# Kernel tuning notes

Hardware: AMD Instinct MI355X
Metric: run time of the kernel (lower is better)

The kernel has to match this reference:

```python
import jax, jax.numpy as jnp
import numpy as np

# dims
B, NB, T, NC = 16, 55, 512, 8          # batch, filter bands, time steps, CSP comps
D, L, H, E, K, F, C = 512, 6, 8, 8, 2, 2048, 2  # embed, depth, heads, experts, top_k, d_ff, classes
DH = D // H
IN = NB * NC  # 440
EPS = 1e-5


def _ln(x, s, b):
    m = x.mean(-1, keepdims=True)
    v = ((x - m) ** 2).mean(-1, keepdims=True)
    return (x - m) / jnp.sqrt(v + EPS) * s + b


def setup_inputs() -> dict:
    key = jax.random.key(0)
    ks = iter(jax.random.split(key, 64))
    n = lambda shape, s=0.02: jax.random.normal(next(ks), shape, jnp.float32) * s
    inp = {
        "x": jax.random.normal(next(ks), (B, NB, T, NC), jnp.float32),
        # frontend
        "proj_w": n((IN, D)), "proj_b": jnp.zeros((D,), jnp.float32),
        "pos": n((1, T, D)),
        "ln_pre_s": jnp.ones((D,), jnp.float32), "ln_pre_b": jnp.zeros((D,), jnp.float32),
        # stacked transformer-block params [L, ...]
        "ln1_s": jnp.ones((L, D), jnp.float32), "ln1_b": jnp.zeros((L, D), jnp.float32),
        "wq": n((L, D, D)), "bq": jnp.zeros((L, D), jnp.float32),
        "wk": n((L, D, D)), "bk": jnp.zeros((L, D), jnp.float32),
        "wv": n((L, D, D)), "bv": jnp.zeros((L, D), jnp.float32),
        "wo": n((L, D, D)), "bo": jnp.zeros((L, D), jnp.float32),
        "ln2_s": jnp.ones((L, D), jnp.float32), "ln2_b": jnp.zeros((L, D), jnp.float32),
        "gate_w": n((L, D, E)),
        "e_w1": n((L, E, D, F)), "e_b1": jnp.zeros((L, E, F), jnp.float32),
        "e_w2": n((L, E, F, D)), "e_b2": jnp.zeros((L, E, D), jnp.float32),
        # classifier head
        "ln_f_s": jnp.ones((D,), jnp.float32), "ln_f_b": jnp.zeros((D,), jnp.float32),
        "head_w": n((D, C)), "head_b": jnp.zeros((C,), jnp.float32),
    }
    return inp


def _moe(h, gw, w1, b1, w2, b2):
    # h: [N, D]; top-K softmax-gated mixture of GELU-FFN experts + load-balance aux loss
    N = h.shape[0]
    probs = jax.nn.softmax(h @ gw, axis=-1)                  # [N, E]
    vals, idx = jax.lax.top_k(probs, K)                      # [N, K]
    w = vals / vals.sum(-1, keepdims=True)                   # renormalized top-k weights
    disp = jax.nn.one_hot(idx, E, dtype=h.dtype)             # [N, K, E]
    combine = (disp * w[..., None]).sum(1)                   # [N, E]
    y = jnp.zeros_like(h)
    for e in range(E):  # small fixed expert loop
        y = y + combine[:, e:e + 1] * (jax.nn.gelu(h @ w1[e] + b1[e]) @ w2[e] + b2[e])
    frac = disp.mean((0, 1)) * K                             # fraction of tokens routed to each expert
    aux = E * jnp.sum(frac * probs.mean(0))
    return y, aux


def reference(x, proj_w, proj_b, pos, ln_pre_s, ln_pre_b, ln1_s, ln1_b, wq, bq, wk, bk,
              wv, bv, wo, bo, ln2_s, ln2_b, gate_w, e_w1, e_b1, e_w2, e_b2,
              ln_f_s, ln_f_b, head_w, head_b):
    b, nb, t, nc = x.shape
    h = x.transpose(0, 2, 1, 3).reshape(b, t, nb * nc) @ proj_w + proj_b  # [B,T,D]
    h = _ln(h + pos[:, :t, :], ln_pre_s, ln_pre_b)
    scale = DH ** -0.5
    total_aux = jnp.float32(0.0)
    for l in range(L):
        # pre-LN multi-head self-attention
        a = _ln(h, ln1_s[l], ln1_b[l])
        q = (a @ wq[l] + bq[l]).reshape(b, t, H, DH)
        k = (a @ wk[l] + bk[l]).reshape(b, t, H, DH)
        v = (a @ wv[l] + bv[l]).reshape(b, t, H, DH)
        att = jax.nn.softmax(jnp.einsum('bqhd,bkhd->bhqk', q, k) * scale, axis=-1)
        o = jnp.einsum('bhqk,bkhd->bqhd', att, v).reshape(b, t, D) @ wo[l] + bo[l]
        h = h + o
        # pre-LN MoE FFN
        m = _ln(h, ln2_s[l], ln2_b[l]).reshape(b * t, D)
        y, aux = _moe(m, gate_w[l], e_w1[l], e_b1[l], e_w2[l], e_b2[l])
        h = h + y.reshape(b, t, D)
        total_aux = total_aux + aux
    pooled = h.mean(axis=1)                                   # [B, D]
    logits = _ln(pooled, ln_f_s, ln_f_b) @ head_w + head_b    # [B, C]
    return logits, total_aux
```

## Files before the change

### kernel.cpp

```cpp
#include <hip/hip_runtime.h>
#include <stdint.h>

typedef unsigned short u16;
typedef unsigned int   u32;
typedef short bh8 __attribute__((ext_vector_type(8)));
typedef float f4  __attribute__((ext_vector_type(4)));

#define NTOK    8192
#define PADROWS 17408
#define MAXTILES 136

__device__ __forceinline__ u16 f2bf(float f){
  u32 u = __float_as_uint(f);
  return (u16)((u + 0x7fffu + ((u>>16)&1u)) >> 16);
}
__device__ __forceinline__ float bf2f(u16 h){ return __uint_as_float(((u32)h)<<16); }
__device__ __forceinline__ u32 pk2(float a, float b){ return (u32)f2bf(a) | ((u32)f2bf(b)<<16); }
__device__ __forceinline__ float gelu_f(float x){
  float u = 0.7978845608028654f*(x + 0.044715f*x*x*x);
  float t = 1.f - 2.f/(__expf(2.f*u)+1.f);
  return 0.5f*x*(1.f+t);
}
__device__ __forceinline__ void gload_lds16(const void* g, void* l){
  __builtin_amdgcn_global_load_lds((const __attribute__((address_space(1))) u32*)g,
                                   (__attribute__((address_space(3))) u32*)l, 16, 0, 0);
}

__global__ __launch_bounds__(256) void xpose_k(const float* __restrict__ x, u16* __restrict__ xt){
  int idx = blockIdx.x*256 + threadIdx.x;
  const float* src = x + (size_t)idx*8;
  float4 a = *(const float4*)src;
  float4 b = *(const float4*)(src+4);
  int t  = idx & 511;
  int nb = (idx>>9) % 55;
  int bb = (idx>>9) / 55;
  uint4 u;
  u.x = pk2(a.x,a.y); u.y = pk2(a.z,a.w); u.z = pk2(b.x,b.y); u.w = pk2(b.z,b.w);
  *(uint4*)&xt[((size_t)(bb*512+t))*448 + nb*8] = u;
}

__device__ __forceinline__ void tile_xpose(const float* __restrict__ src, u16* __restrict__ dst,
                                           int Ksrc, int N, int Kdst, float (*tile)[65])
{
  int tid = threadIdx.x;
  int k0 = blockIdx.y*64, n0 = blockIdx.x*64;
  #pragma unroll
  for (int p=0;p<4;++p){
    int r = p*16 + (tid>>4);
    int c4 = (tid&15)*4;
    int k = k0 + r;
    float4 v = (k < Ksrc) ? *(const float4*)&src[(size_t)k*N + n0 + c4] : (float4){0.f,0.f,0.f,0.f};
    tile[r][c4]=v.x; tile[r][c4+1]=v.y; tile[r][c4+2]=v.z; tile[r][c4+3]=v.w;
  }
  __syncthreads();
  #pragma unroll
  for (int p=0;p<2;++p){
    int rn = p*32 + (tid>>3);
    int ck = (tid&7)*8;
    uint4 u;
    u.x = pk2(tile[ck+0][rn], tile[ck+1][rn]);
    u.y = pk2(tile[ck+2][rn], tile[ck+3][rn]);
    u.z = pk2(tile[ck+4][rn], tile[ck+5][rn]);
    u.w = pk2(tile[ck+6][rn], tile[ck+7][rn]);
    *(uint4*)&dst[(size_t)(n0+rn)*Kdst + k0 + ck] = u;
  }
}

__global__ __launch_bounds__(256) void wconv_k(const float* __restrict__ src, u16* __restrict__ dst,
                                               int Ksrc, int N, int Kdst){
  __shared__ float tile[64][65];
  src += (size_t)blockIdx.z*Ksrc*N;
  dst += (size_t)blockIdx.z*N*Kdst;
  tile_xpose(src, dst, Ksrc, N, Kdst, tile);
}

__global__ __launch_bounds__(256) void wconvqkvo_k(const float* __restrict__ wq, const float* __restrict__ wk,
    const float* __restrict__ wv, const float* __restrict__ wo,
    u16* __restrict__ qkvt, u16* __restrict__ wot)
{
  __shared__ float tile[64][65];
  int z = blockIdx.z;
  int l = z>>2, which = z&3;
  const float* src = ((which==0)? wq : (which==1)? wk : (which==2)? wv : wo) + (size_t)l*512*512;
  u16* dst = (which==3) ? wot + (size_t)l*512*512
                        : qkvt + (size_t)l*1536*512 + (size_t)which*512*512;
  tile_xpose(src, dst, 512, 512, 512, tile);
}

__global__ __launch_bounds__(256) void qkvb_k(const float* __restrict__ bq, const float* __restrict__ bk,
                                              const float* __restrict__ bv, float* __restrict__ qkvb){
  int idx = blockIdx.x*256 + threadIdx.x;
  int l = idx/1536, c = idx - l*1536;
  const float* s = (c<512)? bq : (c<1024)? bk : bv;
  qkvb[idx] = s[l*512 + (c&511)];
}

template<int MODE, bool GATHER>
__global__ __launch_bounds__(256) void gemm2_k(
    const u16* __restrict__ A, int lda,
    const u16* __restrict__ Bt, int ldb, int Ksteps,
    const float* __restrict__ biasBase,
    float* __restrict__ Cf, u16* __restrict__ Cb, int ldc,
    const int* __restrict__ tile_e, const int* __restrict__ toklist,
    const float* __restrict__ wlist, int expN)
{
  __shared__ __align__(16) u16 SMEM[17408];
  u16* As_ = SMEM;
  u16* Bs_ = SMEM + 8192;
  const int tid = threadIdx.x, lane = tid&63, w = tid>>6;
  const int wr = w>>1, wc = w&1;
  int nx = gridDim.x;
  int nwg = nx * gridDim.y;
  int lin = blockIdx.y*nx + blockIdx.x;
  int qq = nwg>>3, rr = nwg&7, xc = lin&7, oo = lin>>3;
  int wg = (xc<rr ? xc*(qq+1) : rr*(qq+1)+(xc-rr)*qq) + oo;
  int by = wg/nx, bx = wg - by*nx;
  const int n0 = bx*128, m0 = by*128;
  const u16* Bp = Bt;
  const float* bias = biasBase;
  if constexpr (MODE>=3){
    int e = tile_e[by];
    Bp   += (size_t)e*(size_t)expN*(size_t)ldb;
    bias += (size_t)e*(size_t)expN;
  }
  const u16* asrc0; const u16* asrc1; const u16* bsrc0; const u16* bsrc1;
  {
    int idx0 = tid, row0 = idx0>>2, sp0 = idx0&3, ks0 = sp0 ^ ((row0>>1)&3);
    int idx1 = 256+tid, row1 = idx1>>2, sp1 = idx1&3, ks1 = sp1 ^ ((row1>>1)&3);
    size_t ar0 = GATHER ? (size_t)toklist[m0+row0] : (size_t)(m0+row0);
    size_t ar1 = GATHER ? (size_t)toklist[m0+row1] : (size_t)(m0+row1);
    asrc0 = A + ar0*(size_t)lda + ks0*8;
    asrc1 = A + ar1*(size_t)lda + ks1*8;
    bsrc0 = Bp + (size_t)(n0+row0)*ldb + ks0*8;
    bsrc1 = Bp + (size_t)(n0+row1)*ldb + ks1*8;
  }
  f4 acc[4][4];
  #pragma unroll
  for (int i=0;i<4;++i)
    #pragma unroll
    for (int j=0;j<4;++j) acc[i][j] = (f4){0.f,0.f,0.f,0.f};

  gload_lds16(asrc0, &As_[tid*8]);
  gload_lds16(asrc1, &As_[(256+tid)*8]);
  gload_lds16(bsrc0, &Bs_[tid*8]);
  gload_lds16(bsrc1, &Bs_[(256+tid)*8]);
  asrc0 += 32; asrc1 += 32; bsrc0 += 32; bsrc1 += 32;
  __syncthreads();

  int buf = 0;
  for (int kt=0; kt<Ksteps; ++kt){
    if (kt+1 < Ksteps){
      int nb = buf^1;
      gload_lds16(asrc0, &As_[nb*4096 + tid*8]);
      gload_lds16(asrc1, &As_[nb*4096 + (256+tid)*8]);
      gload_lds16(bsrc0, &Bs_[nb*4096 + tid*8]);
      gload_lds16(bsrc1, &Bs_[nb*4096 + (256+tid)*8]);
      asrc0 += 32; asrc1 += 32; bsrc0 += 32; bsrc1 += 32;
    }
    bh8 af[4], bf[4];
    const int q = lane>>4;
    #pragma unroll
    for (int mf=0;mf<4;++mf){
      int r = wr*64 + mf*16 + (lane&15);
      af[mf] = *(const bh8*)&As_[buf*4096 + r*32 + (q ^ ((r>>1)&3))*8];
    }
    #pragma unroll
    for (int nf=0;nf<4;++nf){
      int r = wc*64 + nf*16 + (lane&15);
      bf[nf] = *(const bh8*)&Bs_[buf*4096 + r*32 + (q ^ ((r>>1)&3))*8];
    }
    #pragma unroll
    for (int mf=0;mf<4;++mf)
      #pragma unroll
      for (int nf=0;nf<4;++nf)
        acc[mf][nf] = __builtin_amdgcn_mfma_f32_16x16x32_bf16(af[mf], bf[nf], acc[mf][nf], 0, 0, 0);
    __syncthreads();
    buf ^= 1;
  }
  if constexpr (MODE==1 || MODE==3 || MODE==4){
    u16* Cs = SMEM;
    #pragma unroll
    for (int mf=0;mf<4;++mf){
      int row0 = wr*64 + mf*16 + (lane>>4)*4;
      float wl[4];
      if constexpr (MODE==4){
        #pragma unroll
        for (int r=0;r<4;++r) wl[r] = wlist[m0+row0+r];
      }
      #pragma unroll
      for (int nf=0;nf<4;++nf){
        f4 d = acc[mf][nf];
        int col = wc*64 + nf*16 + (lane&15);
        float bv = bias[n0+col];
        #pragma unroll
        for (int r=0;r<4;++r){
          float val = d[r] + bv;
          if constexpr (MODE==3) val = gelu_f(val);
          if constexpr (MODE==4) val = wl[r]*val;
          Cs[(row0+r)*136 + col] = f2bf(val);
        }
      }
    }
    __syncthreads();
    #pragma unroll
    for (int p=0;p<8;++p){
      int idx = p*256 + tid;
      int row = idx>>4, c4 = idx&15;
      bh8 v = *(const bh8*)&Cs[row*136 + c4*8];
      int mrow = m0 + row;
      if constexpr (MODE==1){
        int nc = n0 + c4*8;
        int slab = nc>>6, dh = nc&63;
        *(bh8*)&Cb[((size_t)slab*NTOK + (size_t)mrow)*64 + dh] = v;
      } else {
        *(bh8*)&Cb[(size_t)mrow*ldc + n0 + c4*8] = v;
      }
    }
  } else {
    #pragma unroll
    for (int mf=0;mf<4;++mf){
      #pragma unroll
      for (int nf=0;nf<4;++nf){
        f4 d = acc[mf][nf];
        int ncol = n0 + wc*64 + nf*16 + (lane&15);
        float bv = bias[ncol];
        #pragma unroll
        for (int r=0;r<4;++r){
          int mrow = m0 + wr*64 + mf*16 + (lane>>4)*4 + r;
          float val = d[r] + bv;
          if constexpr (MODE==0){
            Cf[(size_t)mrow*ldc + ncol] = val;
          } else {
            Cf[(size_t)mrow*ldc + ncol] += val;
          }
        }
      }
    }
  }
}

template<bool ADDPOS, bool OUTF32>
__global__ __launch_bounds__(256) void ln_k(const float* __restrict__ X, const float* __restrict__ pos,
    const float* __restrict__ sc, const float* __restrict__ bi,
    float* __restrict__ outF, u16* __restrict__ outB)
{
  int tid=threadIdx.x, lane=tid&63, w=tid>>6;
  int row = blockIdx.x*4 + w;
  const float* xr = X + (size_t)row*512 + lane*8;
  float x[8];
  float4 v0 = *(const float4*)xr;
  float4 v1 = *(const float4*)(xr+4);
  x[0]=v0.x;x[1]=v0.y;x[2]=v0.z;x[3]=v0.w;x[4]=v1.x;x[5]=v1.y;x[6]=v1.z;x[7]=v1.w;
  if constexpr (ADDPOS){
    const float* pr = pos + (size_t)(row&511)*512 + lane*8;
    float4 p0 = *(const float4*)pr, p1 = *(const float4*)(pr+4);
    x[0]+=p0.x;x[1]+=p0.y;x[2]+=p0.z;x[3]+=p0.w;x[4]+=p1.x;x[5]+=p1.y;x[6]+=p1.z;x[7]+=p1.w;
  }
  float sm=0.f, sq=0.f;
  #pragma unroll
  for (int i=0;i<8;++i){ sm+=x[i]; sq+=x[i]*x[i]; }
  #pragma unroll
  for (int mk=1; mk<64; mk<<=1){ sm += __shfl_xor(sm, mk); sq += __shfl_xor(sq, mk); }
  float mean = sm*(1.f/512.f);
  float var  = sq*(1.f/512.f) - mean*mean;
  float rstd = rsqrtf(var + 1e-5f);
  int d0 = lane*8;
  float4 s0 = *(const float4*)(sc+d0), s1 = *(const float4*)(sc+d0+4);
  float4 b0 = *(const float4*)(bi+d0), b1 = *(const float4*)(bi+d0+4);
  float y[8];
  y[0]=(x[0]-mean)*rstd*s0.x+b0.x; y[1]=(x[1]-mean)*rstd*s0.y+b0.y;
  y[2]=(x[2]-mean)*rstd*s0.z+b0.z; y[3]=(x[3]-mean)*rstd*s0.w+b0.w;
  y[4]=(x[4]-mean)*rstd*s1.x+b1.x; y[5]=(x[5]-mean)*rstd*s1.y+b1.y;
  y[6]=(x[6]-mean)*rstd*s1.z+b1.z; y[7]=(x[7]-mean)*rstd*s1.w+b1.w;
  if constexpr (OUTF32){
    float4 o0 = {y[0],y[1],y[2],y[3]}, o1 = {y[4],y[5],y[6],y[7]};
    *(float4*)(outF + (size_t)row*512 + d0)     = o0;
    *(float4*)(outF + (size_t)row*512 + d0 + 4) = o1;
  } else {
    uint4 u; u.x=pk2(y[0],y[1]); u.y=pk2(y[2],y[3]); u.z=pk2(y[4],y[5]); u.w=pk2(y[6],y[7]);
    *(uint4*)&outB[(size_t)row*512 + d0] = u;
  }
}

__global__ __launch_bounds__(256) void gatherln_k(float* __restrict__ h,
    const u16* __restrict__ yb, const int* __restrict__ t2pos,
    const float* __restrict__ sc, const float* __restrict__ bi, u16* __restrict__ outB)
{
  int tid=threadIdx.x, lane=tid&63, w=tid>>6;
  int row = blockIdx.x*4 + w;
  float* hp = h + (size_t)row*512 + lane*8;
  float4 v0 = *(float4*)hp, v1 = *(float4*)(hp+4);
  int p0 = t2pos[2*row], p1 = t2pos[2*row+1];
  uint4 ya = *(const uint4*)&yb[(size_t)p0*512 + lane*8];
  uint4 yv = *(const uint4*)&yb[(size_t)p1*512 + lane*8];
  float x[8];
  x[0]=v0.x + bf2f((u16)(ya.x&0xffff)) + bf2f((u16)(yv.x&0xffff));
  x[1]=v0.y + bf2f((u16)(ya.x>>16))    + bf2f((u16)(yv.x>>16));
  x[2]=v0.z + bf2f((u16)(ya.y&0xffff)) + bf2f((u16)(yv.y&0xffff));
  x[3]=v0.w + bf2f((u16)(ya.y>>16))    + bf2f((u16)(yv.y>>16));
  x[4]=v1.x + bf2f((u16)(ya.z&0xffff)) + bf2f((u16)(yv.z&0xffff));
  x[5]=v1.y + bf2f((u16)(ya.z>>16))    + bf2f((u16)(yv.z>>16));
  x[6]=v1.z + bf2f((u16)(ya.w&0xffff)) + bf2f((u16)(yv.w&0xffff));
  x[7]=v1.w + bf2f((u16)(ya.w>>16))    + bf2f((u16)(yv.w>>16));
  float4 o0 = {x[0],x[1],x[2],x[3]}, o1 = {x[4],x[5],x[6],x[7]};
  *(float4*)hp = o0; *(float4*)(hp+4) = o1;
  float sm=0.f, sq=0.f;
  #pragma unroll
  for (int i=0;i<8;++i){ sm+=x[i]; sq+=x[i]*x[i]; }
  #pragma unroll
  for (int mk=1; mk<64; mk<<=1){ sm += __shfl_xor(sm, mk); sq += __shfl_xor(sq, mk); }
  float mean = sm*(1.f/512.f);
  float rstd = rsqrtf(sq*(1.f/512.f) - mean*mean + 1e-5f);
  int d0 = lane*8;
  float4 s0 = *(const float4*)(sc+d0), s1 = *(const float4*)(sc+d0+4);
  float4 b0 = *(const float4*)(bi+d0), b1 = *(const float4*)(bi+d0+4);
  float y[8];
  y[0]=(x[0]-mean)*rstd*s0.x+b0.x; y[1]=(x[1]-mean)*rstd*s0.y+b0.y;
  y[2]=(x[2]-mean)*rstd*s0.z+b0.z; y[3]=(x[3]-mean)*rstd*s0.w+b0.w;
  y[4]=(x[4]-mean)*rstd*s1.x+b1.x; y[5]=(x[5]-mean)*rstd*s1.y+b1.y;
  y[6]=(x[6]-mean)*rstd*s1.z+b1.z; y[7]=(x[7]-mean)*rstd*s1.w+b1.w;
  uint4 u; u.x=pk2(y[0],y[1]); u.y=pk2(y[2],y[3]); u.z=pk2(y[4],y[5]); u.w=pk2(y[6],y[7]);
  *(uint4*)&outB[(size_t)row*512 + d0] = u;
}

__global__ __launch_bounds__(256) void attn_k(const u16* __restrict__ QKV, u16* __restrict__ Og)
{
  __shared__ __align__(16) u16 VT[2][64*72];
  __shared__ __align__(16) u16 PS[4][16*72];
  int tid=threadIdx.x, lane=tid&63, w=tid>>6;
  int qt=blockIdx.x, hh=blockIdx.y, bb=blockIdx.z;
  const u16* Qh = QKV + ((size_t)hh     *NTOK + (size_t)bb*512)*64;
  const u16* Kh = QKV + ((size_t)(8+hh) *NTOK + (size_t)bb*512)*64;
  const u16* Vh = QKV + ((size_t)(16+hh)*NTOK + (size_t)bb*512)*64;
  size_t obase = (size_t)bb*512*512 + (size_t)hh*64;
  int qrow0 = qt*64 + w*16;
  bh8 qf[2];
  #pragma unroll
  for (int kf=0;kf<2;++kf)
    qf[kf] = *(const bh8*)&Qh[ (size_t)(qrow0 + (lane&15))*64 + kf*32 + (lane>>4)*8 ];
  f4 oacc[4];
  #pragma unroll
  for (int i=0;i<4;++i) oacc[i] = (f4){0.f,0.f,0.f,0.f};
  float mrun[4] = {-1e30f,-1e30f,-1e30f,-1e30f};
  float lrun[4] = {0.f,0.f,0.f,0.f};
  const float scale = 0.125f;

  for (int kt=0; kt<8; ++kt){
    const int buf = kt&1;
    #pragma unroll
    for (int r2=0;r2<2;++r2){
      int idx = r2*256 + tid;
      int dhg = idx&7;
      int dh0 = dhg*8, key = idx>>3;
      uint4 raw = *(const uint4*)&Vh[ (size_t)(kt*64+key)*64 + dh0 ];
      int kx = key ^ (dhg<<3);
      u32 rw[4] = {raw.x, raw.y, raw.z, raw.w};
      #pragma unroll
      for (int j=0;j<4;++j){
        VT[buf][(dh0+2*j  )*72 + kx] = (u16)(rw[j]&0xffff);
        VT[buf][(dh0+2*j+1)*72 + kx] = (u16)(rw[j]>>16);
      }
    }
    f4 s[4];
    #pragma unroll
    for (int nf=0;nf<4;++nf){
      size_t krow = (size_t)(kt*64+nf*16+(lane&15))*64 + (lane>>4)*8;
      bh8 k0 = *(const bh8*)&Kh[krow];
      bh8 k1 = *(const bh8*)&Kh[krow+32];
      f4 z = (f4){0.f,0.f,0.f,0.f};
      z = __builtin_amdgcn_mfma_f32_16x16x32_bf16(qf[0], k0, z, 0,0,0);
      z = __builtin_amdgcn_mfma_f32_16x16x32_bf16(qf[1], k1, z, 0,0,0);
      s[nf] = z;
    }
    float pe[4][4];
    #pragma unroll
    for (int r=0;r<4;++r){
      float sv0=s[0][r]*scale, sv1=s[1][r]*scale, sv2=s[2][r]*scale, sv3=s[3][r]*scale;
      float mt = fmaxf(fmaxf(sv0,sv1), fmaxf(sv2,sv3));
      #pragma unroll
      for (int mk=1; mk<16; mk<<=1) mt = fmaxf(mt, __shfl_xor(mt, mk));
      float mn = fmaxf(mrun[r], mt);
      float sf = __expf(mrun[r]-mn);
      float p0=__expf(sv0-mn), p1=__expf(sv1-mn), p2=__expf(sv2-mn), p3=__expf(sv3-mn);
      pe[0][r]=p0; pe[1][r]=p1; pe[2][r]=p2; pe[3][r]=p3;
      float rs = p0+p1+p2+p3;
      #pragma unroll
      for (int mk=1; mk<16; mk<<=1) rs += __shfl_xor(rs, mk);
      lrun[r] = lrun[r]*sf + rs;
      mrun[r] = mn;
      #pragma unroll
      for (int df=0;df<4;++df) oacc[df][r] *= sf;
    }
    #pragma unroll
    for (int nf=0;nf<4;++nf)
      #pragma unroll
      for (int r=0;r<4;++r)
        PS[w][ ((lane>>4)*4+r)*72 + nf*16 + (lane&15) ] = f2bf(pe[nf][r]);
    __syncthreads();
    #pragma unroll
    for (int ks=0;ks<2;++ks){
      bh8 pa = *(const bh8*)&PS[w][ (lane&15)*72 + ks*32 + (lane>>4)*8 ];
      #pragma unroll
      for (int df=0;df<4;++df){
        int dh = df*16 + (lane&15);
        int sgrp = (dh>>3)&7;
        bh8 vb = *(const bh8*)&VT[buf][ dh*72 + ((ks*4 + (lane>>4)) ^ sgrp)*8 ];
        oacc[df] = __builtin_amdgcn_mfma_f32_16x16x32_bf16(pa, vb, oacc[df], 0,0,0);
      }
    }
  }
  #pragma unroll
  for (int df=0;df<4;++df)
    #pragma unroll
    for (int r=0;r<4;++r){
      int qr = qrow0 + (lane>>4)*4 + r;
      float ov = oacc[df][r] / lrun[r];
      Og[ obase + (size_t)qr*512 + df*16 + (lane&15) ] = f2bf(ov);
    }
}

__global__ __launch_bounds__(256) void lnroute_k(const float* __restrict__ h,
    const float* __restrict__ sc, const float* __restrict__ bi, u16* __restrict__ outB,
    const float* __restrict__ gw,
    float* __restrict__ psum, int* __restrict__ cnt, int* __restrict__ t2e, float* __restrict__ t2w)
{
  __shared__ float ps[8]; __shared__ int cs[8];
  int tid=threadIdx.x, lane=tid&63, w=tid>>6;
  if (tid<8){ ps[tid]=0.f; cs[tid]=0; }
  __syncthreads();
  int d0 = lane*8;
  float4 s0 = *(const float4*)(sc+d0), s1 = *(const float4*)(sc+d0+4);
  float4 b0 = *(const float4*)(bi+d0), b1 = *(const float4*)(bi+d0+4);
  for (int it=0; it<4; ++it){
    int t = blockIdx.x*16 + w*4 + it;
    const float* xr = h + (size_t)t*512 + d0;
    float x[8];
    float4 v0 = *(const float4*)xr, v1 = *(const float4*)(xr+4);
    x[0]=v0.x;x[1]=v0.y;x[2]=v0.z;x[3]=v0.w;x[4]=v1.x;x[5]=v1.y;x[6]=v1.z;x[7]=v1.w;
    float sm=0.f, sq=0.f;
    #pragma unroll
    for (int i=0;i<8;++i){ sm+=x[i]; sq+=x[i]*x[i]; }
    #pragma unroll
    for (int mk=1; mk<64; mk<<=1){ sm += __shfl_xor(sm, mk); sq += __shfl_xor(sq, mk); }
    float mean = sm*(1.f/512.f);
    float rstd = rsqrtf(sq*(1.f/512.f) - mean*mean + 1e-5f);
    float y[8];
    y[0]=(x[0]-mean)*rstd*s0.x+b0.x; y[1]=(x[1]-mean)*rstd*s0.y+b0.y;
    y[2]=(x[2]-mean)*rstd*s0.z+b0.z; y[3]=(x[3]-mean)*rstd*s0.w+b0.w;
    y[4]=(x[4]-mean)*rstd*s1.x+b1.x; y[5]=(x[5]-mean)*rstd*s1.y+b1.y;
    y[6]=(x[6]-mean)*rstd*s1.z+b1.z; y[7]=(x[7]-mean)*rstd*s1.w+b1.w;
    uint4 u; u.x=pk2(y[0],y[1]); u.y=pk2(y[2],y[3]); u.z=pk2(y[4],y[5]); u.w=pk2(y[6],y[7]);
    *(uint4*)&outB[(size_t)t*512 + d0] = u;
    float acc[8] = {0,0,0,0,0,0,0,0};
    #pragma unroll
    for (int j=0;j<8;++j){
      const float* g = gw + (size_t)(d0+j)*8;
      float4 g0 = *(const float4*)g, g1 = *(const float4*)(g+4);
      acc[0]+=y[j]*g0.x; acc[1]+=y[j]*g0.y; acc[2]+=y[j]*g0.z; acc[3]+=y[j]*g0.w;
      acc[4]+=y[j]*g1.x; acc[5]+=y[j]*g1.y; acc[6]+=y[j]*g1.z; acc[7]+=y[j]*g1.w;
    }
    #pragma unroll
    for (int mk=1; mk<64; mk<<=1)
      #pragma unroll
      for (int e=0;e<8;++e) acc[e] += __shfl_xor(acc[e], mk);
    if (lane==0){
      float mx=acc[0];
      #pragma unroll
      for (int e=1;e<8;++e) mx = fmaxf(mx, acc[e]);
      float pe[8], tot=0.f;
      #pragma unroll
      for (int e=0;e<8;++e){ pe[e]=__expf(acc[e]-mx); tot+=pe[e]; }
      float inv = 1.f/tot;
      #pragma unroll
      for (int e=0;e<8;++e) pe[e]*=inv;
      int e0=0; float v0e=pe[0];
      #pragma unroll
      for (int e=1;e<8;++e) if (pe[e]>v0e){ v0e=pe[e]; e0=e; }
      int e1=-1; float v1e=-1.f;
      #pragma unroll
      for (int e=0;e<8;++e) if (e!=e0 && pe[e]>v1e){ v1e=pe[e]; e1=e; }
      float invw = 1.f/(v0e+v1e);
      t2e[2*t]=e0; t2w[2*t]=v0e*invw; t2e[2*t+1]=e1; t2w[2*t+1]=v1e*invw;
      #pragma unroll
      for (int e=0;e<8;++e) atomicAdd(&ps[e], pe[e]);
      atomicAdd(&cs[e0],1); atomicAdd(&cs[e1],1);
    }
  }
  __syncthreads();
  if (tid<8){ atomicAdd(&psum[tid], ps[tid]); atomicAdd(&cnt[tid], cs[tid]); }
}

__global__ __launch_bounds__(256) void offsets_k(const int* __restrict__ cnt, const float* __restrict__ psum,
    int* __restrict__ offs, int* __restrict__ fill, int* __restrict__ tile_e,
    int* __restrict__ toklist, float* __restrict__ wlist, float* __restrict__ auxp)
{
  int tid = threadIdx.x, b = blockIdx.x;
  int i = b*256 + tid;
  if (i < PADROWS){ toklist[i]=0; wlist[i]=0.f; }
  if (b==0){
    if (tid==0){
      int off=0; float auxl=0.f;
      for (int e=0;e<8;++e){
        offs[e] = off;
        int reg = (cnt[e]+127)&~127;
        int t0 = off>>7, t1 = (off+reg)>>7;
        for (int t=t0;t<t1;++t) tile_e[t]=e;
        off += reg;
        auxl += ((float)cnt[e]*(1.f/8192.f)) * (psum[e]*(1.f/8192.f));
      }
      for (int t=off>>7; t<MAXTILES; ++t) tile_e[t]=0;
      auxp[0] += 8.f*auxl;
    }
    if (tid<8) fill[tid]=0;
  }
}

__global__ __launch_bounds__(256) void scatter_k(const int* __restrict__ t2e, const float* __restrict__ t2w,
    const int* __restrict__ offs, int* __restrict__ fill,
    int* __restrict__ toklist, float* __restrict__ wlist, int* __restrict__ t2pos)
{
  int t = blockIdx.x*256 + threadIdx.x;
  #pragma unroll
  for (int kk=0;kk<2;++kk){
    int e = t2e[2*t+kk];
    int p = atomicAdd(&fill[e], 1);
    int i = offs[e] + p;
    toklist[i] = t; wlist[i] = t2w[2*t+kk]; t2pos[2*t+kk] = i;
  }
}

__global__ __launch_bounds__(256) void gather_k(float* __restrict__ h, const u16* __restrict__ yb,
                                                const int* __restrict__ t2pos)
{
  int tid = threadIdx.x;
  int t = blockIdx.x*4 + (tid>>6);
  int lane = tid&63;
  int p0 = t2pos[2*t], p1 = t2pos[2*t+1];
  uint4 a = *(const uint4*)&yb[(size_t)p0*512 + lane*8];
  uint4 b = *(const uint4*)&yb[(size_t)p1*512 + lane*8];
  float* hp = h + (size_t)t*512 + lane*8;
  float4 h0 = *(float4*)hp, h1 = *(float4*)(hp+4);
  h0.x += bf2f((u16)(a.x&0xffff)) + bf2f((u16)(b.x&0xffff));
  h0.y += bf2f((u16)(a.x>>16))    + bf2f((u16)(b.x>>16));
  h0.z += bf2f((u16)(a.y&0xffff)) + bf2f((u16)(b.y&0xffff));
  h0.w += bf2f((u16)(a.y>>16))    + bf2f((u16)(b.y>>16));
  h1.x += bf2f((u16)(a.z&0xffff)) + bf2f((u16)(b.z&0xffff));
  h1.y += bf2f((u16)(a.z>>16))    + bf2f((u16)(b.z>>16));
  h1.z += bf2f((u16)(a.w&0xffff)) + bf2f((u16)(b.w&0xffff));
  h1.w += bf2f((u16)(a.w>>16))    + bf2f((u16)(b.w>>16));
  *(float4*)hp = h0; *(float4*)(hp+4) = h1;
}

__global__ __launch_bounds__(256) void pool_k(const float* __restrict__ h, float* __restrict__ pooled){
  int idx = blockIdx.x*256 + threadIdx.x;
  int bb = idx>>9, d = idx&511;
  const float* p = h + (size_t)bb*512*512 + d;
  float s=0.f;
  for (int t=0;t<512;++t) s += p[(size_t)t*512];
  pooled[idx] = s*(1.f/512.f);
}

__global__ __launch_bounds__(256) void head_k(const float* __restrict__ pooled,
    const float* __restrict__ sc, const float* __restrict__ bi,
    const float* __restrict__ hw, const float* __restrict__ hb,
    const float* __restrict__ auxp, float* __restrict__ out)
{
  int tid=threadIdx.x, lane=tid&63, w=tid>>6;
  for (int i=0;i<4;++i){
    int row = w*4+i;
    const float* xr = pooled + (size_t)row*512 + lane*8;
    float x[8];
    float4 v0 = *(const float4*)xr, v1 = *(const float4*)(xr+4);
    x[0]=v0.x;x[1]=v0.y;x[2]=v0.z;x[3]=v0.w;x[4]=v1.x;x[5]=v1.y;x[6]=v1.z;x[7]=v1.w;
    float sm=0.f, sq=0.f;
    #pragma unroll
    for (int j=0;j<8;++j){ sm+=x[j]; sq+=x[j]*x[j]; }
    #pragma unroll
    for (int mk=1; mk<64; mk<<=1){ sm += __shfl_xor(sm, mk); sq += __shfl_xor(sq, mk); }
    float mean = sm*(1.f/512.f);
    float rstd = rsqrtf(sq*(1.f/512.f) - mean*mean + 1e-5f);
    int d0 = lane*8;
    float c0=0.f, c1=0.f;
    #pragma unroll
    for (int j=0;j<8;++j){
      float yv = (x[j]-mean)*rstd*sc[d0+j] + bi[d0+j];
      c0 += yv*hw[(d0+j)*2]; c1 += yv*hw[(d0+j)*2+1];
    }
    #pragma unroll
    for (int mk=1; mk<64; mk<<=1){ c0 += __shfl_xor(c0, mk); c1 += __shfl_xor(c1, mk); }
    if (lane==0){ out[row*2+0] = c0 + hb[0]; out[row*2+1] = c1 + hb[1]; }
  }
  if (tid==0) out[32] = auxp[0];
}

extern "C" void kernel_launch(void* const* d_in, const int* in_sizes, int n_in,
                              void* d_out, int out_size, void* d_ws, size_t ws_size,
                              hipStream_t stream)
{
  (void)in_sizes; (void)n_in; (void)out_size; (void)ws_size;
  const float* x      = (const float*)d_in[0];
  const float* proj_w = (const float*)d_in[1];
  const float* proj_b = (const float*)d_in[2];
  const float* pos    = (const float*)d_in[3];
  const float* ln_pre_s=(const float*)d_in[4];
  const float* ln_pre_b=(const float*)d_in[5];
  const float* ln1_s  = (const float*)d_in[6];
  const float* ln1_b  = (const float*)d_in[7];
  const float* wq     = (const float*)d_in[8];
  const float* bq     = (const float*)d_in[9];
  const float* wk     = (const float*)d_in[10];
  const float* bk     = (const float*)d_in[11];
  const float* wv     = (const float*)d_in[12];
  const float* bv     = (const float*)d_in[13];
  const float* wo     = (const float*)d_in[14];
  const float* bo     = (const float*)d_in[15];
  const float* ln2_s  = (const float*)d_in[16];
  const float* ln2_b  = (const float*)d_in[17];
  const float* gate_w = (const float*)d_in[18];
  const float* e_w1   = (const float*)d_in[19];
  const float* e_b1   = (const float*)d_in[20];
  const float* e_w2   = (const float*)d_in[21];
  const float* e_b2   = (const float*)d_in[22];
  const float* ln_f_s = (const float*)d_in[23];
  const float* ln_f_b = (const float*)d_in[24];
  const float* head_w = (const float*)d_in[25];
  const float* head_b = (const float*)d_in[26];

  char* base = (char*)d_ws;
  size_t off = 0;
  auto carve = [&](size_t bytes)->char*{
    char* r = base + off; off += (bytes + 255) & ~(size_t)255; return r;
  };
  u16*   xt      = (u16*)  carve((size_t)8192*448*2);
  float* h       = (float*)carve((size_t)8192*512*4);
  u16*   a       = (u16*)  carve((size_t)8192*512*2);
  u16*   qkv     = (u16*)  carve((size_t)8192*1536*2);
  u16*   ob      = (u16*)  carve((size_t)8192*512*2);
  u16*   hidden  = (u16*)  carve((size_t)PADROWS*2048*2);
  u16*   ybuf    = (u16*)  carve((size_t)PADROWS*512*2);
  u16*   projt   = (u16*)  carve((size_t)512*448*2);
  u16*   qkvt    = (u16*)  carve((size_t)6*1536*512*2);
  u16*   wot     = (u16*)  carve((size_t)6*512*512*2);
  u16*   w1t     = (u16*)  carve((size_t)6*8*2048*512*2);
  u16*   w2t     = (u16*)  carve((size_t)6*8*512*2048*2);
  float* qkvb    = (float*)carve((size_t)6*1536*4);
  int*   toklist = (int*)  carve(PADROWS*4);
  float* wlist   = (float*)carve(PADROWS*4);
  int*   tile_e  = (int*)  carve(256*4);
  int*   rcntA   = (int*)  carve(6*16*4);
  int*   fill    = (int*)  carve(64);
  int*   offs    = (int*)  carve(64);
  int*   t2e     = (int*)  carve(16384*4);
  float* t2w     = (float*)carve(16384*4);
  int*   t2pos   = (int*)  carve(16384*4);
  float* pooled  = (float*)carve(8192*4);
  float* auxp    = (float*)carve(256);

  hipMemsetAsync(xt, 0, (size_t)8192*448*2, stream);
  hipMemsetAsync(rcntA, 0, 6*16*4, stream);
  hipMemsetAsync(auxp, 0, 4, stream);

  xpose_k<<<1760, 256, 0, stream>>>(x, xt);
  wconv_k<<<dim3(8,7,1), 256, 0, stream>>>(proj_w, projt, 440, 512, 448);
  wconvqkvo_k<<<dim3(8,8,24), 256, 0, stream>>>(wq, wk, wv, wo, qkvt, wot);
  wconv_k<<<dim3(32,8,48), 256, 0, stream>>>(e_w1, w1t, 512, 2048, 512);
  wconv_k<<<dim3(8,32,48), 256, 0, stream>>>(e_w2, w2t, 2048, 512, 2048);
  qkvb_k<<<36, 256, 0, stream>>>(bq, bk, bv, qkvb);
  gemm2_k<0,false><<<dim3(4,64), 256, 0, stream>>>(xt, 448, projt, 448, 14, proj_b,
      h, nullptr, 512, nullptr, nullptr, nullptr, 0);
  ln_k<true,true><<<2048, 256, 0, stream>>>(h, pos, ln_pre_s, ln_pre_b, h, nullptr);

  for (int l=0; l<6; ++l){
    int*   cnt  = rcntA + l*16;
    float* psum = (float*)(cnt + 8);
    if (l == 0)
      ln_k<false,false><<<2048, 256, 0, stream>>>(h, nullptr, ln1_s, ln1_b, nullptr, a);
    else
      gatherln_k<<<2048, 256, 0, stream>>>(h, ybuf, t2pos,
          ln1_s+(size_t)l*512, ln1_b+(size_t)l*512, a);
    gemm2_k<1,false><<<dim3(12,64), 256, 0, stream>>>(a, 512, qkvt+(size_t)l*1536*512, 512, 16,
        qkvb+(size_t)l*1536, nullptr, qkv, 1536, nullptr, nullptr, nullptr, 0);
    attn_k<<<dim3(8,8,16), 256, 0, stream>>>(qkv, ob);
    gemm2_k<2,false><<<dim3(4,64), 256, 0, stream>>>(ob, 512, wot+(size_t)l*512*512, 512, 16,
        bo+(size_t)l*512, h, nullptr, 512, nullptr, nullptr, nullptr, 0);
    lnroute_k<<<512, 256, 0, stream>>>(h, ln2_s+(size_t)l*512, ln2_b+(size_t)l*512, a,
        gate_w+(size_t)l*512*8, psum, cnt, t2e, t2w);
    offsets_k<<<68, 256, 0, stream>>>(cnt, psum, offs, fill, tile_e, toklist, wlist, auxp);
    scatter_k<<<32, 256, 0, stream>>>(t2e, t2w, offs, fill, toklist, wlist, t2pos);
    gemm2_k<3,true ><<<dim3(16,MAXTILES), 256, 0, stream>>>(a, 512, w1t+(size_t)l*8*2048*512, 512, 16,
        e_b1 + (size_t)l*8*2048, nullptr, hidden, 2048, tile_e, toklist, wlist, 2048);
    gemm2_k<4,false><<<dim3(4,MAXTILES), 256, 0, stream>>>(hidden, 2048, w2t+(size_t)l*8*512*2048, 2048, 64,
        e_b2 + (size_t)l*8*512, nullptr, ybuf, 512, tile_e, nullptr, wlist, 512);
  }

  gather_k<<<2048, 256, 0, stream>>>(h, ybuf, t2pos);
  pool_k<<<32, 256, 0, stream>>>(h, pooled);
  head_k<<<1, 256, 0, stream>>>(pooled, ln_f_s, ln_f_b, head_w, head_b, auxp, (float*)d_out);
}
```

Measured before the change: 2.185 ms.

## Switch GEMM k-loop to three-stage LDS pipeline with explicit vmcnt waits

```diff
diff --git a/kernel.cpp b/kernel.cpp
--- a/kernel.cpp
+++ b/kernel.cpp
@@ -104,9 +104,7 @@
     const int* __restrict__ tile_e, const int* __restrict__ toklist,
     const float* __restrict__ wlist, int expN)
 {
-  __shared__ __align__(16) u16 SMEM[17408];
-  u16* As_ = SMEM;
-  u16* Bs_ = SMEM + 8192;
+  __shared__ __align__(16) u16 SMEM[24576];
   const int tid = threadIdx.x, lane = tid&63, w = tid>>6;
   const int wr = w>>1, wc = w&1;
   int nx = gridDim.x;
@@ -140,44 +138,52 @@
     #pragma unroll
     for (int j=0;j<4;++j) acc[i][j] = (f4){0.f,0.f,0.f,0.f};
 
-  gload_lds16(asrc0, &As_[tid*8]);
-  gload_lds16(asrc1, &As_[(256+tid)*8]);
-  gload_lds16(bsrc0, &Bs_[tid*8]);
-  gload_lds16(bsrc1, &Bs_[(256+tid)*8]);
-  asrc0 += 32; asrc1 += 32; bsrc0 += 32; bsrc1 += 32;
-  __syncthreads();
-
-  int buf = 0;
+  auto STAGE = [&](int kt){
+    u16* bufA = SMEM + (kt%3)*8192;
+    u16* bufB = bufA + 4096;
+    gload_lds16(asrc0 + (size_t)kt*32, &bufA[tid*8]);
+    gload_lds16(asrc1 + (size_t)kt*32, &bufA[2048 + tid*8]);
+    gload_lds16(bsrc0 + (size_t)kt*32, &bufB[tid*8]);
+    gload_lds16(bsrc1 + (size_t)kt*32, &bufB[2048 + tid*8]);
+  };
+
+  STAGE(0);
+  if (Ksteps > 1) STAGE(1);
+  if (Ksteps > 2) STAGE(2);
+
   for (int kt=0; kt<Ksteps; ++kt){
-    if (kt+1 < Ksteps){
-      int nb = buf^1;
-      gload_lds16(asrc0, &As_[nb*4096 + tid*8]);
-      gload_lds16(asrc1, &As_[nb*4096 + (256+tid)*8]);
-      gload_lds16(bsrc0, &Bs_[nb*4096 + tid*8]);
-      gload_lds16(bsrc1, &Bs_[nb*4096 + (256+tid)*8]);
-      asrc0 += 32; asrc1 += 32; bsrc0 += 32; bsrc1 += 32;
-    }
+    int rem = Ksteps - 1 - kt;
+    if (rem >= 2)      asm volatile("s_waitcnt vmcnt(8)" ::: "memory");
+    else if (rem == 1) asm volatile("s_waitcnt vmcnt(4)" ::: "memory");
+    else               asm volatile("s_waitcnt vmcnt(0)" ::: "memory");
+    __builtin_amdgcn_s_barrier();
+    u16* bufA = SMEM + (kt%3)*8192;
+    u16* bufB = bufA + 4096;
     bh8 af[4], bf[4];
     const int q = lane>>4;
     #pragma unroll
     for (int mf=0;mf<4;++mf){
       int r = wr*64 + mf*16 + (lane&15);
-      af[mf] = *(const bh8*)&As_[buf*4096 + r*32 + (q ^ ((r>>1)&3))*8];
+      af[mf] = *(const bh8*)&bufA[r*32 + (q ^ ((r>>1)&3))*8];
     }
     #pragma unroll
     for (int nf=0;nf<4;++nf){
       int r = wc*64 + nf*16 + (lane&15);
-      bf[nf] = *(const bh8*)&Bs_[buf*4096 + r*32 + (q ^ ((r>>1)&3))*8];
-    }
+      bf[nf] = *(const bh8*)&bufB[r*32 + (q ^ ((r>>1)&3))*8];
+    }
+    asm volatile("s_waitcnt lgkmcnt(0)" ::: "memory");
+    __builtin_amdgcn_sched_barrier(0);
+    __builtin_amdgcn_s_barrier();
+    __builtin_amdgcn_sched_barrier(0);
+    if (kt+3 < Ksteps) STAGE(kt+3);
     #pragma unroll
     for (int mf=0;mf<4;++mf)
       #pragma unroll
       for (int nf=0;nf<4;++nf)
         acc[mf][nf] = __builtin_amdgcn_mfma_f32_16x16x32_bf16(af[mf], bf[nf], acc[mf][nf], 0, 0, 0);
+  }
+  if constexpr (MODE==1 || MODE==3 || MODE==4){
     __syncthreads();
-    buf ^= 1;
-  }
-  if constexpr (MODE==1 || MODE==3 || MODE==4){
     u16* Cs = SMEM;
     #pragma unroll
     for (int mf=0;mf<4;++mf){
```

Measured after the change: 2.097 ms. -4.0%, faster.
